# Kernel tuning notes

Hardware: AMD Instinct MI355X
Metric: run time of the kernel (lower is better)

Reference implementation:

```python
import jax, jax.numpy as jnp
import numpy as np

K = 16  # nsample for knn_point

def _bn(x, g, b):
    # inference-mode BatchNorm1d folded to per-channel affine (running stats 0/1)
    return x * g[None, :, None] + b[None, :, None]

def _knn(xyz, k):
    # xyz: [B,3,N] -> idx [B,N,k] of k nearest neighbors (squared L2)
    p = xyz.transpose(0, 2, 1)                                   # [B,N,3]
    sq = jnp.sum(p * p, axis=-1)                                 # [B,N]
    d = sq[:, :, None] + sq[:, None, :] - 2.0 * jnp.einsum('bnc,bmc->bnm', p, p)
    _, idx = jax.lax.top_k(-d, k)
    return idx

def _gather(hT, idx):
    # hT: [B,N,C], idx: [B,N,K] -> [B,N,K,C]
    return jax.vmap(lambda a, i: a[i])(hT, idx)

def setup_inputs():
    key = jax.random.key(0)
    ks = jax.random.split(key, 12)
    B, N, C = 16, 2048, 128
    def w(k, shape, fan):
        return jax.random.normal(k, shape, jnp.float32) * (1.0 / np.sqrt(fan))
    o = jnp.ones; z = jnp.zeros
    return {
        'points': jax.random.normal(ks[0], (B, 6, N), jnp.float32),
        'label': jax.random.uniform(ks[1], (B, 1, 16), jnp.float32),
        'We1': w(ks[2], (C, 6), 6), 'ge1': o(C), 'be1': z(C),
        'We2': w(ks[3], (C, C), C), 'ge2': o(C), 'be2': z(C),
        'W1': w(ks[4], (3, C, C), C), 'g1': o((3, C)), 'b1': z((3, C)),
        'W2': w(ks[5], (3, C, C), C), 'g2': o((3, C)), 'b2': z((3, C)),
        'Wf': w(ks[6], (1024, 3 * C), 3 * C), 'gf': o(1024), 'bf': z(1024),
        'Wl': w(ks[7], (64, 16), 16), 'gl': o(64), 'bl': z(64),
        'Wc1': w(ks[8], (512, 3136), 3136), 'bc1': z(512), 'gc1': o(512), 'bb1': z(512),
        'Wc2': w(ks[9], (256, 512), 512), 'bc2': z(256), 'gc2': o(256), 'bb2': z(256),
        'Wc3': w(ks[10], (50, 256), 256), 'bc3': z(50),
    }

def reference(points, label, We1, ge1, be1, We2, ge2, be2, W1, g1, b1, W2, g2, b2,
              Wf, gf, bf, Wl, gl, bl, Wc1, bc1, gc1, bb1, Wc2, bc2, gc2, bb2, Wc3, bc3):
    B, _, N = points.shape
    x = points[:, :6, :]
    xyz = x[:, :3, :]
    idx = _knn(xyz, K)                                            # [B,N,16]
    # input embedding: two conv1x1 + BN + ReLU
    h = jax.nn.relu(_bn(jnp.einsum('oc,bcn->bon', We1, x), ge1, be1))
    h = jax.nn.relu(_bn(jnp.einsum('oc,bcn->bon', We2, h), ge2, be2))
    xs = []
    for i in range(3):  # PVDSA_Res blocks (simplified: conv-BN-ReLU, kNN max-agg, conv-BN + residual)
        t = jax.nn.relu(_bn(jnp.einsum('oc,bcn->bon', W1[i], h), g1[i], b1[i]))
        nbr = _gather(t.transpose(0, 2, 1), idx)                  # [B,N,K,C]
        m = nbr.max(axis=2).transpose(0, 2, 1)                    # [B,C,N]
        h = jax.nn.relu(_bn(jnp.einsum('oc,bcn->bon', W2[i], m), g2[i], b2[i]) + h)
        xs.append(h)
    xcat = jnp.concatenate(xs, axis=1)                            # [B,384,N]
    xf = jax.nn.leaky_relu(_bn(jnp.einsum('oc,bcn->bon', Wf, xcat), gf, bf), 0.2)  # [B,1024,N]
    x_max = xf.max(axis=-1)                                       # [B,1024]
    x_avg = xf.mean(axis=-1)                                      # [B,1024]
    cls = jnp.broadcast_to(label.transpose(0, 2, 1), (B, 16, N))
    lab = jax.nn.leaky_relu(_bn(jnp.einsum('oc,bcn->bon', Wl, cls), gl, bl), 0.2)  # [B,64,N]
    glob = jnp.concatenate([
        jnp.broadcast_to(x_max[:, :, None], (B, 1024, N)),
        jnp.broadcast_to(x_avg[:, :, None], (B, 1024, N)),
        lab], axis=1)
    xa = jnp.concatenate([xf, glob], axis=1)                      # [B,3136,N]
    c = jax.nn.relu(_bn(jnp.einsum('oc,bcn->bon', Wc1, xa) + bc1[None, :, None], gc1, bb1))
    c = jax.nn.relu(_bn(jnp.einsum('oc,bcn->bon', Wc2, c) + bc2[None, :, None], gc2, bb2))
    out = jnp.einsum('oc,bcn->bon', Wc3, c) + bc3[None, :, None]  # [B,50,N]
    return out
```

## Files before the change

kernel.cpp:

```cpp
#include <hip/hip_runtime.h>
#include <cstdint>
#include <cstddef>

#define DEVINL __device__ __forceinline__

typedef float    f32x4 __attribute__((ext_vector_type(4)));
typedef _Float16 f16x8 __attribute__((ext_vector_type(8)));
typedef _Float16 f16x4 __attribute__((ext_vector_type(4)));

constexpr int BB = 16, NN = 2048, MM = 32768;

constexpr size_t OFF_WE1 = 0;
constexpr size_t OFF_WE2 = OFF_WE1 + 128 * 64 * 2;
constexpr size_t OFF_W1  = OFF_WE2 + 128 * 128 * 2;
constexpr size_t OFF_W2  = OFF_W1  + 3 * 128 * 128 * 2;
constexpr size_t OFF_WF  = OFF_W2  + 3 * 128 * 128 * 2;
constexpr size_t OFF_WC1 = OFF_WF  + 1024 * 384 * 2;
constexpr size_t OFF_WC2 = OFF_WC1 + 512 * 1024 * 2;
constexpr size_t OFF_WC3 = OFF_WC2 + 256 * 512 * 2;
constexpr size_t OFF_BC2 = OFF_WC3 + 128 * 256 * 2;
constexpr size_t OFF_BC3 = OFF_BC2 + 256 * 4;
constexpr size_t OFF_CVEC= OFF_BC3 + 128 * 4;
constexpr size_t OFF_PMAX= OFF_CVEC+ 16 * 512 * 4;
constexpr size_t OFF_PSUM= OFF_PMAX+ 16 * 16 * 1024 * 4;
constexpr size_t OFF_IDX = OFF_PSUM+ 16 * 16 * 1024 * 4;
constexpr size_t OFF_R1  = 8ull << 20;
constexpr size_t OFF_X0  = OFF_R1;
constexpr size_t OFF_HT  = OFF_R1 + (4ull  << 20);
constexpr size_t OFF_TT  = OFF_R1 + (12ull << 20);
constexpr size_t OFF_MT  = OFF_R1 + (20ull << 20);
constexpr size_t OFF_C1  = OFF_R1;
constexpr size_t OFF_XCAT= OFF_R1 + (32ull << 20);
constexpr size_t OFF_C2  = OFF_XCAT;
constexpr size_t OFF_XF  = OFF_XCAT + (24ull << 20);

__global__ __launch_bounds__(256) void fold_all_kernel(
    const float* We1, const float* ge1, const float* We2, const float* ge2,
    const float* W1,  const float* g1,  const float* W2,  const float* g2,
    const float* Wf,  const float* gf,  const float* Wc1, const float* gc1,
    const float* Wc2, const float* gc2, const float* Wc3,
    const float* gc2b, const float* bc2, const float* bb2, const float* bc3,
    const float* pts, char* ws)
{
    const int bid = blockIdx.x;
    const int tid = threadIdx.x;

    if (bid == 4704) {
        ((float*)(ws + OFF_BC2))[tid] = gc2b[tid] * bc2[tid] + bb2[tid];
        return;
    }
    if (bid == 4705) {
        if (tid < 128) ((float*)(ws + OFF_BC3))[tid] = (tid < 50) ? bc3[tid] : 0.f;
        return;
    }
    if (bid >= 4706) {
        int m = (bid - 4706) * 256 + tid;
        int b = m >> 11, n = m & 2047;
        const float* ps = pts + (size_t)b * 6 * 2048 + n;
        _Float16 tmp[64];
#pragma unroll
        for (int c = 0; c < 64; ++c) tmp[c] = (_Float16)0.f;
#pragma unroll
        for (int c = 0; c < 6; ++c) tmp[c] = (_Float16)ps[(size_t)c << 11];
        _Float16* dst = (_Float16*)(ws + OFF_X0) + (size_t)m * 64;
#pragma unroll
        for (int v = 0; v < 8; ++v) *(f16x8*)(dst + v * 8) = *(const f16x8*)(tmp + v * 8);
        return;
    }

    int id, base;
    if      (bid < 32)   { id = 0;  base = 0;    }
    else if (bid < 96)   { id = 1;  base = 32;   }
    else if (bid < 160)  { id = 2;  base = 96;   }
    else if (bid < 224)  { id = 3;  base = 160;  }
    else if (bid < 288)  { id = 4;  base = 224;  }
    else if (bid < 352)  { id = 5;  base = 288;  }
    else if (bid < 416)  { id = 6;  base = 352;  }
    else if (bid < 480)  { id = 7;  base = 416;  }
    else if (bid < 2016) { id = 8;  base = 480;  }
    else if (bid < 4064) { id = 9;  base = 2016; }
    else if (bid < 4576) { id = 10; base = 4064; }
    else                 { id = 11; base = 4576; }

    const float* src = nullptr; const float* g = nullptr; _Float16* dst = nullptr;
    int O = 0, K = 0, lds = 0, Kp = 0;
    switch (id) {
        case 0:  src = We1; g = ge1; O = 128; K = 6;    lds = 6;    Kp = 64;   dst = (_Float16*)(ws + OFF_WE1); break;
        case 1:  src = We2; g = ge2; O = 128; K = 128;  lds = 128;  Kp = 128;  dst = (_Float16*)(ws + OFF_WE2); break;
        case 2: case 3: case 4: {
            int i = id - 2;
            src = W1 + (size_t)i * 16384; g = g1 + i * 128; O = 128; K = 128; lds = 128; Kp = 128;
            dst = (_Float16*)(ws + OFF_W1) + (size_t)i * 16384; break; }
        case 5: case 6: case 7: {
            int i = id - 5;
            src = W2 + (size_t)i * 16384; g = g2 + i * 128; O = 128; K = 128; lds = 128; Kp = 128;
            dst = (_Float16*)(ws + OFF_W2) + (size_t)i * 16384; break; }
        case 8:  src = Wf;  g = gf;  O = 1024; K = 384;  lds = 384;  Kp = 384;  dst = (_Float16*)(ws + OFF_WF);  break;
        case 9:  src = Wc1; g = gc1; O = 512;  K = 1024; lds = 3136; Kp = 1024; dst = (_Float16*)(ws + OFF_WC1); break;
        case 10: src = Wc2; g = gc2; O = 256;  K = 512;  lds = 512;  Kp = 512;  dst = (_Float16*)(ws + OFF_WC2); break;
        default: src = Wc3; g = nullptr; O = 50; K = 256; lds = 256; Kp = 256;  dst = (_Float16*)(ws + OFF_WC3); break;
    }
    int e = (bid - base) * 256 + tid;
    int o = e / Kp, k = e - o * Kp;
    float v = 0.f;
    if (o < O && k < K) {
        v = src[(size_t)o * lds + k];
        if (g) v *= g[o];
    }
    dst[e] = (_Float16)v;
}

DEVINL float knn_dist(const float4 pq, const float4 pm) {
    float t = pq.x * pm.x;
    t = fmaf(pq.y, pm.y, t);
    t = fmaf(pq.z, pm.z, t);
    return fmaf(-2.f, t, pm.w);
}

#define KNN_DINS(X) do { \
    const float x_ = (X); \
    d15 = __builtin_amdgcn_fmed3f(x_, d14, d15); \
    d14 = __builtin_amdgcn_fmed3f(x_, d13, d14); \
    d13 = __builtin_amdgcn_fmed3f(x_, d12, d13); \
    d12 = __builtin_amdgcn_fmed3f(x_, d11, d12); \
    d11 = __builtin_amdgcn_fmed3f(x_, d10, d11); \
    d10 = __builtin_amdgcn_fmed3f(x_, d9,  d10); \
    d9  = __builtin_amdgcn_fmed3f(x_, d8,  d9);  \
    d8  = __builtin_amdgcn_fmed3f(x_, d7,  d8);  \
    d7  = __builtin_amdgcn_fmed3f(x_, d6,  d7);  \
    d6  = __builtin_amdgcn_fmed3f(x_, d5,  d6);  \
    d5  = __builtin_amdgcn_fmed3f(x_, d4,  d5);  \
    d4  = __builtin_amdgcn_fmed3f(x_, d3,  d4);  \
    d3  = __builtin_amdgcn_fmed3f(x_, d2,  d3);  \
    d2  = __builtin_amdgcn_fmed3f(x_, d1,  d2);  \
    d1  = __builtin_amdgcn_fmed3f(x_, d0,  d1);  \
    d0  = __builtin_amdgcn_fmed3f(x_, -3.4e38f, d0); \
} while (0)

#define KNN_CE(A, B) { const float lo_ = fminf(A, B), hi_ = fmaxf(A, B); A = lo_; B = hi_; }

#define KNN_MERGE(OFF) do { \
    const float n0  = __shfl_xor(d0,  OFF), n1  = __shfl_xor(d1,  OFF), \
                n2  = __shfl_xor(d2,  OFF), n3  = __shfl_xor(d3,  OFF), \
                n4  = __shfl_xor(d4,  OFF), n5  = __shfl_xor(d5,  OFF), \
                n6  = __shfl_xor(d6,  OFF), n7  = __shfl_xor(d7,  OFF), \
                n8  = __shfl_xor(d8,  OFF), n9  = __shfl_xor(d9,  OFF), \
                n10 = __shfl_xor(d10, OFF), n11 = __shfl_xor(d11, OFF), \
                n12 = __shfl_xor(d12, OFF), n13 = __shfl_xor(d13, OFF), \
                n14 = __shfl_xor(d14, OFF), n15 = __shfl_xor(d15, OFF); \
    d0  = fminf(d0,  n15); d1  = fminf(d1,  n14); d2  = fminf(d2,  n13); d3  = fminf(d3,  n12); \
    d4  = fminf(d4,  n11); d5  = fminf(d5,  n10); d6  = fminf(d6,  n9);  d7  = fminf(d7,  n8);  \
    d8  = fminf(d8,  n7);  d9  = fminf(d9,  n6);  d10 = fminf(d10, n5);  d11 = fminf(d11, n4);  \
    d12 = fminf(d12, n3);  d13 = fminf(d13, n2);  d14 = fminf(d14, n1);  d15 = fminf(d15, n0);  \
    KNN_CE(d0, d8)  KNN_CE(d1, d9)  KNN_CE(d2, d10) KNN_CE(d3, d11) \
    KNN_CE(d4, d12) KNN_CE(d5, d13) KNN_CE(d6, d14) KNN_CE(d7, d15) \
    KNN_CE(d0, d4)  KNN_CE(d1, d5)  KNN_CE(d2, d6)  KNN_CE(d3, d7)  \
    KNN_CE(d8, d12) KNN_CE(d9, d13) KNN_CE(d10,d14) KNN_CE(d11,d15) \
    KNN_CE(d0, d2)  KNN_CE(d1, d3)  KNN_CE(d4, d6)  KNN_CE(d5, d7)  \
    KNN_CE(d8, d10) KNN_CE(d9, d11) KNN_CE(d12,d14) KNN_CE(d13,d15) \
    KNN_CE(d0, d1)  KNN_CE(d2, d3)  KNN_CE(d4, d5)  KNN_CE(d6, d7)  \
    KNN_CE(d8, d9)  KNN_CE(d10,d11) KNN_CE(d12,d13) KNN_CE(d14,d15) \
} while (0)

__global__ __launch_bounds__(256) void knn_kernel(const float* __restrict__ pts, int* __restrict__ idxout)
{
    __shared__ float4 P[2048];
    __shared__ unsigned short buf[32][96];
    __shared__ int cnt[32];
    __shared__ int wcnt[32];
    const int tid = threadIdx.x;
    const int b = blockIdx.x;
    const float* pb = pts + (size_t)b * 6 * 2048;
    for (int i = tid; i < 2048; i += 256) {
        float x = pb[i];
        float y = pb[2048 + i];
        float z = pb[4096 + i];
        P[i] = make_float4(x, y, z, x * x + y * y + z * z);
    }
    if (tid < 32) { cnt[tid] = 0; wcnt[tid] = 0; }
    __syncthreads();

    const int p = tid & 7;
    const int g = tid >> 3;
    const int q = blockIdx.y * 32 + g;
    const float4 pq = P[q];

    float d0 = 3.4e38f, d1 = 3.4e38f, d2 = 3.4e38f, d3 = 3.4e38f;
#pragma unroll 4
    for (int it = 0; it < 256; ++it) {
        const float4 pm = P[it * 8 + p];
        const float x = knn_dist(pq, pm);
        d3 = __builtin_amdgcn_fmed3f(x, d2, d3);
        d2 = __builtin_amdgcn_fmed3f(x, d1, d2);
        d1 = __builtin_amdgcn_fmed3f(x, d0, d1);
        d0 = fminf(x, d0);
    }
    float d4 = 3.4e38f, d5 = 3.4e38f, d6 = 3.4e38f, d7 = 3.4e38f,
          d8 = 3.4e38f, d9 = 3.4e38f, d10 = 3.4e38f, d11 = 3.4e38f,
          d12 = 3.4e38f, d13 = 3.4e38f, d14 = 3.4e38f, d15 = 3.4e38f;
    KNN_MERGE(1);
    KNN_MERGE(2);
    KNN_MERGE(4);
    const float tub = d15;

#pragma unroll 4
    for (int it = 0; it < 256; ++it) {
        const int m = it * 8 + p;
        const float d = knn_dist(pq, P[m]);
        if (d <= tub) {
            const int pos = atomicAdd(&cnt[g], 1);
            if (pos < 96) buf[g][pos] = (unsigned short)m;
        }
    }
    int C = cnt[g];
    if (C > 96) C = 96;

    d0 = 3.4e38f; d1 = 3.4e38f; d2 = 3.4e38f; d3 = 3.4e38f;
    d4 = 3.4e38f; d5 = 3.4e38f; d6 = 3.4e38f; d7 = 3.4e38f;
    d8 = 3.4e38f; d9 = 3.4e38f; d10 = 3.4e38f; d11 = 3.4e38f;
    d12 = 3.4e38f; d13 = 3.4e38f; d14 = 3.4e38f; d15 = 3.4e38f;
    for (int j = p; j < C; j += 8) {
        const int m = buf[g][j];
        const float x = knn_dist(pq, P[m]);
        KNN_DINS(x);
    }
    KNN_MERGE(1);
    KNN_MERGE(2);
    KNN_MERGE(4);
    const float t = d15;

    int* op = idxout + (((size_t)(b << 11) + q) << 4);
    for (int j = p; j < C; j += 8) {
        const int m = buf[g][j];
        const float d = knn_dist(pq, P[m]);
        if (d <= t) {
            const int pos = atomicAdd(&wcnt[g], 1);
            if (pos < 16) op[pos] = m;
        }
    }
}

template<int TM>
__global__ __launch_bounds__(256) void gemm_tile(
    const _Float16* __restrict__ W, const _Float16* __restrict__ X,
    _Float16* __restrict__ Y, float* __restrict__ Y32,
    const float* __restrict__ bias, const _Float16* __restrict__ Res,
    int Kp, int ldX, int xoff, int ldY, int yoff, int Opad,
    int act, int biasPerBatch, int ldR, int roff, int Olimit,
    float* __restrict__ pmax, float* __restrict__ psum)
{
    constexpr int MI = TM / 32;
    constexpr int ASZ = 128 * 64;
    constexpr int BSZ = TM * 64;
    __shared__ _Float16 SH[2 * (ASZ + BSZ)];

    const int tid  = threadIdx.x;
    const int lane = tid & 63, wave = tid >> 6;
    const int r = lane & 15, quad = lane >> 4;
    const int m_blk = blockIdx.x * TM, o_blk = blockIdx.y * 128;
    const int oh = (wave >> 1) * 64, mh = (wave & 1) * (TM / 2);

    f32x4 acc[4][MI];
#pragma unroll
    for (int a = 0; a < 4; ++a)
#pragma unroll
        for (int c = 0; c < MI; ++c) acc[a][c] = (f32x4){0.f, 0.f, 0.f, 0.f};

    const int srow  = wave * 8 + (lane >> 3);
    const int sslot = lane & 7;

    auto STAGE = [&](int bufi, int k0) {
        _Float16* As = SH + bufi * (ASZ + BSZ);
        _Float16* Bs = As + ASZ;
#pragma unroll
        for (int t = 0; t < 4; ++t) {
            const int rowA = t * 32 + srow;
            const int gk = k0 + ((sslot ^ (rowA & 7)) << 3);
            const _Float16* gA = W + (size_t)(o_blk + rowA) * Kp + gk;
            __builtin_amdgcn_global_load_lds(
                (const __attribute__((address_space(1))) unsigned int*)gA,
                (__attribute__((address_space(3))) unsigned int*)(As + t * 2048 + wave * 512),
                16, 0, 0);
        }
#pragma unroll
        for (int t = 0; t < TM / 32; ++t) {
            const int rowB = t * 32 + srow;
            const int gk = k0 + ((sslot ^ (rowB & 7)) << 3);
            const _Float16* gB = X + (size_t)(m_blk + rowB) * ldX + xoff + gk;
            __builtin_amdgcn_global_load_lds(
                (const __attribute__((address_space(1))) unsigned int*)gB,
                (__attribute__((address_space(3))) unsigned int*)(Bs + t * 2048 + wave * 512),
                16, 0, 0);
        }
    };

    const int nt = Kp >> 6;
    STAGE(0, 0);
    int cur = 0;
    for (int t = 0; t < nt; ++t) {
        if (t + 1 < nt) {
            STAGE(cur ^ 1, (t + 1) << 6);
            if constexpr (TM == 128) asm volatile("s_waitcnt vmcnt(8)" ::: "memory");
            else                     asm volatile("s_waitcnt vmcnt(6)" ::: "memory");
        } else {
            asm volatile("s_waitcnt vmcnt(0)" ::: "memory");
        }
        __builtin_amdgcn_sched_barrier(0);
        __builtin_amdgcn_s_barrier();
        asm volatile("" ::: "memory");

        const _Float16* As = SH + cur * (ASZ + BSZ);
        const _Float16* Bs = As + ASZ;
        __builtin_amdgcn_s_setprio(1);
#pragma unroll
        for (int ks = 0; ks < 2; ++ks) {
            f16x8 af[4], bf[MI];
#pragma unroll
            for (int oi = 0; oi < 4; ++oi) {
                const int row = oh + oi * 16 + r;
                const int slot = (ks * 4 + quad) ^ (row & 7);
                af[oi] = *(const f16x8*)(As + row * 64 + slot * 8);
            }
#pragma unroll
            for (int mi = 0; mi < MI; ++mi) {
                const int row = mh + mi * 16 + r;
                const int slot = (ks * 4 + quad) ^ (row & 7);
                bf[mi] = *(const f16x8*)(Bs + row * 64 + slot * 8);
            }
#pragma unroll
            for (int oi = 0; oi < 4; ++oi)
#pragma unroll
                for (int mi = 0; mi < MI; ++mi)
                    acc[oi][mi] = __builtin_amdgcn_mfma_f32_16x16x32_f16(af[oi], bf[mi], acc[oi][mi], 0, 0, 0);
        }
        __builtin_amdgcn_s_setprio(0);
        asm volatile("" ::: "memory");
        __builtin_amdgcn_s_barrier();
        cur ^= 1;
    }

    const int bb = biasPerBatch ? (m_blk >> 11) * Opad : 0;
    __syncthreads();

    if (Y32) {
#pragma unroll
        for (int oi = 0; oi < 4; ++oi) {
            const int og = o_blk + oh + oi * 16 + quad * 4;
            const f32x4 bv = *(const f32x4*)(bias + bb + og);
#pragma unroll
            for (int mi = 0; mi < MI; ++mi) {
                const int m = m_blk + mh + mi * 16 + r;
                const int bidx = m >> 11, n = m & 2047;
                f32x4 v = acc[oi][mi] + bv;
#pragma unroll
                for (int j = 0; j < 4; ++j) {
                    float x = v[j];
                    if (act == 1)      x = (x > 0.f) ? x : 0.0f;
                    else if (act == 2) x = (x > 0.f) ? x : 0.2f * x;
                    const int o = og + j;
                    if (o < Olimit)
                        Y32[((size_t)(bidx * 50 + o) << 11) + n] = x;
                }
            }
        }
        return;
    }

    _Float16* OT = SH;
#pragma unroll
    for (int oi = 0; oi < 4; ++oi) {
        const int ol = oh + oi * 16 + quad * 4;
        const f32x4 bv = *(const f32x4*)(bias + bb + o_blk + ol);
#pragma unroll
        for (int mi = 0; mi < MI; ++mi) {
            const int row = mh + mi * 16 + r;
            f32x4 v = acc[oi][mi] + bv;
            if (Res) {
                f16x4 rr = *(const f16x4*)(Res + (size_t)(m_blk + row) * ldR + roff + o_blk + ol);
#pragma unroll
                for (int j = 0; j < 4; ++j) v[j] += (float)rr[j];
            }
            f16x4 ov;
#pragma unroll
            for (int j = 0; j < 4; ++j) {
                float x = v[j];
                if (act == 1)      x = (x > 0.f) ? x : 0.0f;
                else if (act == 2) x = (x > 0.f) ? x : 0.2f * x;
                ov[j] = (_Float16)x;
            }
            const int s = ((ol >> 2) ^ (row & 31)) << 2;
            *(f16x4*)(OT + row * 128 + s) = ov;
        }
    }
    __syncthreads();
#pragma unroll
    for (int it2 = 0; it2 < TM / 16; ++it2) {
        const int row = it2 * 16 + (tid >> 4);
        const int c = tid & 15;
        const int s0 = ((c * 2) ^ (row & 31)) << 2;
        const int s1 = ((c * 2 + 1) ^ (row & 31)) << 2;
        f16x4 a = *(const f16x4*)(OT + row * 128 + s0);
        f16x4 b2 = *(const f16x4*)(OT + row * 128 + s1);
        f16x8 o8;
        o8[0] = a[0]; o8[1] = a[1]; o8[2] = a[2]; o8[3] = a[3];
        o8[4] = b2[0]; o8[5] = b2[1]; o8[6] = b2[2]; o8[7] = b2[3];
        *(f16x8*)(Y + (size_t)(m_blk + row) * ldY + yoff + o_blk + c * 8) = o8;
    }

    if constexpr (TM == 128) {
        if (pmax) {
            const int cg = tid & 31, h = tid >> 5;
            float mx0 = -3.4e38f, mx1 = -3.4e38f, mx2 = -3.4e38f, mx3 = -3.4e38f;
            float sm0 = 0.f, sm1 = 0.f, sm2 = 0.f, sm3 = 0.f;
#pragma unroll
            for (int rr = 0; rr < 16; ++rr) {
                const int r2 = h * 16 + rr;
                const f16x4 v = *(const f16x4*)(OT + r2 * 128 + ((cg ^ (r2 & 31)) << 2));
                const float x0 = (float)v[0], x1 = (float)v[1], x2 = (float)v[2], x3 = (float)v[3];
                mx0 = fmaxf(mx0, x0); sm0 += x0;
                mx1 = fmaxf(mx1, x1); sm1 += x1;
                mx2 = fmaxf(mx2, x2); sm2 += x2;
                mx3 = fmaxf(mx3, x3); sm3 += x3;
            }
            __syncthreads();
            float* PR = (float*)SH;
            float* pw = PR + (size_t)(h * 128 + cg * 4) * 2;
            pw[0] = mx0; pw[1] = sm0; pw[2] = mx1; pw[3] = sm1;
            pw[4] = mx2; pw[5] = sm2; pw[6] = mx3; pw[7] = sm3;
            __syncthreads();
            if (tid < 128) {
                float M = -3.4e38f, S = 0.f;
#pragma unroll
                for (int h2 = 0; h2 < 8; ++h2) {
                    M = fmaxf(M, PR[(size_t)(h2 * 128 + tid) * 2]);
                    S += PR[(size_t)(h2 * 128 + tid) * 2 + 1];
                }
                const int b2 = m_blk >> 11, mt = (m_blk >> 7) & 15;
                pmax[((size_t)(b2 * 16 + mt) << 10) + o_blk + tid] = M;
                psum[((size_t)(b2 * 16 + mt) << 10) + o_blk + tid] = S;
            }
        }
    }
}

typedef short s16x8 __attribute__((ext_vector_type(8)));
__global__ __launch_bounds__(256) void gather_max_kernel(
    const short* __restrict__ T, const int* __restrict__ idx, short* __restrict__ Mo)
{
    const int tid = threadIdx.x;
    const int p = blockIdx.x * 16 + (tid >> 4);
    const int l = tid & 15;
    const int b = p >> 11;
    const int* ip = idx + (size_t)p * 16;
    size_t row = (size_t)((b << 11) + ip[0]);
    s16x8 cur = *(const s16x8*)(T + row * 128 + l * 8);
    unsigned short best[8];
#pragma unroll
    for (int e = 0; e < 8; ++e) best[e] = (unsigned short)cur[e];
#pragma unroll
    for (int j = 1; j < 16; ++j) {
        row = (size_t)((b << 11) + ip[j]);
        s16x8 v = *(const s16x8*)(T + row * 128 + l * 8);
#pragma unroll
        for (int e = 0; e < 8; ++e) {
            unsigned short u = (unsigned short)v[e];
            if (u > best[e]) best[e] = u;
        }
    }
    s16x8 ov;
#pragma unroll
    for (int e = 0; e < 8; ++e) ov[e] = (short)best[e];
    *(s16x8*)(Mo + (size_t)p * 128 + l * 8) = ov;
}

__global__ __launch_bounds__(256) void cvec_kernel(
    const float* __restrict__ label, const float* __restrict__ Wl, const float* __restrict__ gl, const float* __restrict__ bl,
    const float* __restrict__ Wc1, const float* __restrict__ bc1, const float* __restrict__ gc1, const float* __restrict__ bb1,
    const float* __restrict__ pmax, const float* __restrict__ psum, float* __restrict__ cvec)
{
    __shared__ float v[2112];
    __shared__ float red[256];
    const int b = blockIdx.x, og = blockIdx.y, tid = threadIdx.x;
    for (int i = tid; i < 1024; i += 256) {
        float mx = -3.4e38f, sm = 0.f;
#pragma unroll
        for (int c = 0; c < 16; ++c) {
            mx = fmaxf(mx, pmax[((size_t)(b * 16 + c) << 10) + i]);
            sm += psum[((size_t)(b * 16 + c) << 10) + i];
        }
        v[i] = mx;
        v[1024 + i] = sm * (1.f / 2048.f);
    }
    if (tid < 64) {
        float s = 0.f;
        for (int i = 0; i < 16; ++i) s += Wl[tid * 16 + i] * label[b * 16 + i];
        s = gl[tid] * s + bl[tid];
        v[2048 + tid] = (s > 0.f) ? s : 0.2f * s;
    }
    __syncthreads();
    const int o = og * 64 + (tid >> 2), part = tid & 3;
    const float* wrow = Wc1 + (size_t)o * 3136 + 1024 + part * 528;
    float s = 0.f;
    for (int j = 0; j < 528; ++j) s += wrow[j] * v[part * 528 + j];
    red[tid] = s;
    __syncthreads();
    if (part == 0) {
        float tot = red[tid] + red[tid + 1] + red[tid + 2] + red[tid + 3];
        cvec[((size_t)b << 9) + o] = gc1[o] * (tot + bc1[o]) + bb1[o];
    }
}

extern "C" void kernel_launch(void* const* d_in, const int* in_sizes, int n_in,
                              void* d_out, int out_size, void* d_ws, size_t ws_size,
                              hipStream_t stream)
{
    (void)in_sizes; (void)n_in; (void)out_size; (void)ws_size;
    const float* points = (const float*)d_in[0];
    const float* label  = (const float*)d_in[1];
    const float* We1 = (const float*)d_in[2];
    const float* ge1 = (const float*)d_in[3];
    const float* be1 = (const float*)d_in[4];
    const float* We2 = (const float*)d_in[5];
    const float* ge2 = (const float*)d_in[6];
    const float* be2 = (const float*)d_in[7];
    const float* W1  = (const float*)d_in[8];
    const float* g1  = (const float*)d_in[9];
    const float* b1  = (const float*)d_in[10];
    const float* W2  = (const float*)d_in[11];
    const float* g2  = (const float*)d_in[12];
    const float* b2  = (const float*)d_in[13];
    const float* Wf  = (const float*)d_in[14];
    const float* gf  = (const float*)d_in[15];
    const float* bfv = (const float*)d_in[16];
    const float* Wl  = (const float*)d_in[17];
    const float* gl  = (const float*)d_in[18];
    const float* bl  = (const float*)d_in[19];
    const float* Wc1 = (const float*)d_in[20];
    const float* bc1 = (const float*)d_in[21];
    const float* gc1 = (const float*)d_in[22];
    const float* bb1 = (const float*)d_in[23];
    const float* Wc2 = (const float*)d_in[24];
    const float* bc2 = (const float*)d_in[25];
    const float* gc2 = (const float*)d_in[26];
    const float* bb2 = (const float*)d_in[27];
    const float* Wc3 = (const float*)d_in[28];
    const float* bc3 = (const float*)d_in[29];

    char* ws = (char*)d_ws;
    _Float16* hT  = (_Float16*)(ws + OFF_HT);
    _Float16* tT  = (_Float16*)(ws + OFF_TT);
    _Float16* mT  = (_Float16*)(ws + OFF_MT);
    _Float16* xct = (_Float16*)(ws + OFF_XCAT);
    _Float16* xf  = (_Float16*)(ws + OFF_XF);
    _Float16* c1  = (_Float16*)(ws + OFF_C1);
    _Float16* c2  = (_Float16*)(ws + OFF_C2);
    int*      idx = (int*)     (ws + OFF_IDX);
    _Float16* x0  = (_Float16*)(ws + OFF_X0);

    _Float16* wE1 = (_Float16*)(ws + OFF_WE1);
    _Float16* wE2 = (_Float16*)(ws + OFF_WE2);
    _Float16* w1f = (_Float16*)(ws + OFF_W1);
    _Float16* w2f = (_Float16*)(ws + OFF_W2);
    _Float16* wF  = (_Float16*)(ws + OFF_WF);
    _Float16* wC1 = (_Float16*)(ws + OFF_WC1);
    _Float16* wC2 = (_Float16*)(ws + OFF_WC2);
    _Float16* wC3 = (_Float16*)(ws + OFF_WC3);
    float* bC2 = (float*)(ws + OFF_BC2);
    float* bC3 = (float*)(ws + OFF_BC3);
    float* cv  = (float*)(ws + OFF_CVEC);
    float* pmx = (float*)(ws + OFF_PMAX);
    float* psm = (float*)(ws + OFF_PSUM);

    fold_all_kernel<<<dim3(4834), 256, 0, stream>>>(We1, ge1, We2, ge2, W1, g1, W2, g2,
                                                    Wf, gf, Wc1, gc1, Wc2, gc2, Wc3,
                                                    gc2, bc2, bb2, bc3, points, ws);
    knn_kernel<<<dim3(BB, NN / 32), 256, 0, stream>>>(points, idx);

    gemm_tile<64><<<dim3(512, 1), 256, 0, stream>>>(wE1, x0, tT, nullptr, be1, nullptr, 64, 64, 0, 128, 0, 128, 1, 0, 0, 0, 128, nullptr, nullptr);
    gemm_tile<64><<<dim3(512, 1), 256, 0, stream>>>(wE2, tT, hT, nullptr, be2, nullptr, 128, 128, 0, 128, 0, 128, 1, 0, 0, 0, 128, nullptr, nullptr);

    for (int i = 0; i < 3; ++i) {
        const _Float16* hin = (i == 0) ? hT : xct;
        int ldH  = (i == 0) ? 128 : 384;
        int offH = (i == 0) ? 0 : (i - 1) * 128;
        gemm_tile<64><<<dim3(512, 1), 256, 0, stream>>>(w1f + (size_t)i * 16384, hin, tT, nullptr, b1 + i * 128, nullptr,
                                                        128, ldH, offH, 128, 0, 128, 1, 0, 0, 0, 128, nullptr, nullptr);
        gather_max_kernel<<<dim3(MM / 16), 256, 0, stream>>>((const short*)tT, idx, (short*)mT);
        gemm_tile<64><<<dim3(512, 1), 256, 0, stream>>>(w2f + (size_t)i * 16384, mT, xct, nullptr, b2 + i * 128, hin,
                                                        128, 128, 0, 384, i * 128, 128, 1, 0, ldH, offH, 128, nullptr, nullptr);
    }

    gemm_tile<128><<<dim3(256, 8), 256, 0, stream>>>(wF, xct, xf, nullptr, bfv, nullptr, 384, 384, 0, 1024, 0, 1024, 2, 0, 0, 0, 1024, pmx, psm);

    cvec_kernel<<<dim3(BB, 8), 256, 0, stream>>>(label, Wl, gl, bl, Wc1, bc1, gc1, bb1, pmx, psm, cv);

    gemm_tile<128><<<dim3(256, 4), 256, 0, stream>>>(wC1, xf, c1, nullptr, cv, nullptr, 1024, 1024, 0, 512, 0, 512, 1, 1, 0, 0, 512, nullptr, nullptr);
    gemm_tile<128><<<dim3(256, 2), 256, 0, stream>>>(wC2, c1, c2, nullptr, bC2, nullptr, 512, 512, 0, 256, 0, 256, 1, 0, 0, 0, 256, nullptr, nullptr);
    gemm_tile<128><<<dim3(256, 1), 256, 0, stream>>>(wC3, c2, nullptr, (float*)d_out, bC3, nullptr, 256, 256, 0, 0, 0, 128, 0, 0, 0, 0, 50, nullptr, nullptr);
}
```

Before: 414.6 us.

## Add 256x256 LDS-pipelined GEMM kernel for the two largest layers

Adds a new 512-thread GEMM kernel with 256x256 output tiles. It loads global memory straight into LDS with a fine-grained double-buffered schedule, explicit vmcnt waits and raised priority around the MFMA work. The kernel is used for the 1024x384 feature layer, including the fused max/sum partial reductions, and for the 512x1024 classifier layer. The larger tiles cut redundant operand traffic and raise MFMA density. In exchange the kernel needs 128KB of LDS per block and gets fewer blocks per GPU (512 and 256), and the partial-reduction layout changes to 8 chunks per batch.

```diff
diff --git a/kernel.cpp b/kernel.cpp
--- a/kernel.cpp
+++ b/kernel.cpp
@@ -240,14 +240,181 @@
     }
 }
 
+__global__ __launch_bounds__(512, 2) void gemm256(
+    const _Float16* __restrict__ W, const _Float16* __restrict__ X,
+    _Float16* __restrict__ Y, const float* __restrict__ bias,
+    int Kp, int ldX, int ldY, int Opad, int act, int biasPerBatch,
+    float* __restrict__ pmax, float* __restrict__ psum)
+{
+    __shared__ _Float16 SH[65536];
+    const int tid  = threadIdx.x;
+    const int lane = tid & 63, wave = tid >> 6;
+    const int r = lane & 15, quad = lane >> 4;
+    const int wo = wave & 3, wm = wave >> 2;
+    const int m_blk = blockIdx.x * 256, o_blk = blockIdx.y * 256;
+    const int nt = Kp >> 6;
+
+    f32x4 acc[4][8];
+#pragma unroll
+    for (int a = 0; a < 4; ++a)
+#pragma unroll
+        for (int c = 0; c < 8; ++c) acc[a][c] = (f32x4){0.f, 0.f, 0.f, 0.f};
+
+    auto STAGE_HALF = [&](int mat, int tile, int h) {
+        const int d = tile & 1;
+        _Float16* base = SH + (size_t)(((d * 2 + mat) * 2 + h) << 13);
+#pragma unroll
+        for (int i = 0; i < 2; ++i) {
+            const int g  = ((wave * 2 + i) << 6) + lane;
+            const int R  = g >> 2, s2 = g & 3;
+            const int K4 = s2 ^ ((R >> 1) & 3);
+            const int gk = (tile << 6) + (h << 5) + (K4 << 3);
+            const _Float16* src = (mat == 0)
+                ? W + (size_t)(o_blk + R) * Kp + gk
+                : X + (size_t)(m_blk + R) * ldX + gk;
+            __builtin_amdgcn_global_load_lds(
+                (const __attribute__((address_space(1))) unsigned int*)src,
+                (__attribute__((address_space(3))) unsigned int*)(base + ((wave * 2 + i) << 9)),
+                16, 0, 0);
+        }
+    };
+
+    STAGE_HALF(0, 0, 0); STAGE_HALF(1, 0, 0);
+    STAGE_HALF(0, 0, 1); STAGE_HALF(1, 0, 1);
+    if (nt > 1) { STAGE_HALF(0, 1, 0); STAGE_HALF(1, 1, 0); }
+
+    f16x8 af[4];
+    for (int t = 0; t < nt; ++t) {
+        const int d = t & 1;
+#pragma unroll
+        for (int ph = 0; ph < 4; ++ph) {
+            const int ks = ph >> 1, mh = ph & 1;
+            if (ph == 0) {
+                if (t == nt - 1) asm volatile("s_waitcnt vmcnt(4)" ::: "memory");
+                else             asm volatile("s_waitcnt vmcnt(8)" ::: "memory");
+            } else if (ph == 2) {
+                if (t == nt - 1) asm volatile("s_waitcnt vmcnt(0)" ::: "memory");
+                else             asm volatile("s_waitcnt vmcnt(8)" ::: "memory");
+            }
+            __builtin_amdgcn_sched_barrier(0);
+            __builtin_amdgcn_s_barrier();
+            __builtin_amdgcn_sched_barrier(0);
+
+            if (mh == 0) {
+#pragma unroll
+                for (int oi = 0; oi < 4; ++oi) {
+                    const int R  = (wo << 6) + (oi << 4) + r;
+                    const int s2 = quad ^ ((R >> 1) & 3);
+                    af[oi] = *(const f16x8*)(SH + (size_t)(((d * 2 + 0) * 2 + ks) << 13)
+                                                + (size_t)(((R << 2) + s2) << 3));
+                }
+            }
+            f16x8 bf[4];
+#pragma unroll
+            for (int j = 0; j < 4; ++j) {
+                const int mi = (mh << 2) + j;
+                const int R  = (wm << 7) + (mi << 4) + r;
+                const int s2 = quad ^ ((R >> 1) & 3);
+                bf[j] = *(const f16x8*)(SH + (size_t)(((d * 2 + 1) * 2 + ks) << 13)
+                                            + (size_t)(((R << 2) + s2) << 3));
+            }
+
+            if (ph == 0)      { if (t + 1 < nt) STAGE_HALF(0, t + 1, 1); }
+            else if (ph == 1) { if (t + 1 < nt) STAGE_HALF(1, t + 1, 1); }
+            else if (ph == 2) { if (t + 2 < nt) STAGE_HALF(0, t + 2, 0); }
+            else              { if (t + 2 < nt) STAGE_HALF(1, t + 2, 0); }
+
+            __builtin_amdgcn_s_setprio(1);
+#pragma unroll
+            for (int oi = 0; oi < 4; ++oi)
+#pragma unroll
+                for (int j = 0; j < 4; ++j)
+                    acc[oi][(mh << 2) + j] =
+                        __builtin_amdgcn_mfma_f32_16x16x32_f16(af[oi], bf[j], acc[oi][(mh << 2) + j], 0, 0, 0);
+            __builtin_amdgcn_s_setprio(0);
+            __builtin_amdgcn_sched_barrier(0);
+        }
+    }
+    __syncthreads();
+
+    const int bb = biasPerBatch ? (m_blk >> 11) * Opad : 0;
+    _Float16* OT = SH;
+#pragma unroll
+    for (int oi = 0; oi < 4; ++oi) {
+        const int ol = (wo << 6) + (oi << 4) + (quad << 2);
+        const f32x4 bv = *(const f32x4*)(bias + bb + o_blk + ol);
+#pragma unroll
+        for (int mi = 0; mi < 8; ++mi) {
+            const int row = (wm << 7) + (mi << 4) + r;
+            f32x4 v = acc[oi][mi] + bv;
+            f16x4 ov;
+#pragma unroll
+            for (int j = 0; j < 4; ++j) {
+                float x = v[j];
+                if (act == 1)      x = (x > 0.f) ? x : 0.0f;
+                else if (act == 2) x = (x > 0.f) ? x : 0.2f * x;
+                ov[j] = (_Float16)x;
+            }
+            const int s = (ol >> 2) ^ (row & 31);
+            *(f16x4*)(OT + row * 256 + s * 4) = ov;
+        }
+    }
+    __syncthreads();
+#pragma unroll
+    for (int p2 = 0; p2 < 16; ++p2) {
+        const int g = (p2 << 9) + tid;
+        const int row = g >> 5, c = g & 31;
+        const int s0 = ((c << 1)) ^ (row & 31);
+        const int s1 = ((c << 1) | 1) ^ (row & 31);
+        f16x4 a  = *(const f16x4*)(OT + row * 256 + s0 * 4);
+        f16x4 b2 = *(const f16x4*)(OT + row * 256 + s1 * 4);
+        f16x8 o8;
+        o8[0] = a[0]; o8[1] = a[1]; o8[2] = a[2]; o8[3] = a[3];
+        o8[4] = b2[0]; o8[5] = b2[1]; o8[6] = b2[2]; o8[7] = b2[3];
+        *(f16x8*)(Y + (size_t)(m_blk + row) * ldY + o_blk + (c << 3)) = o8;
+    }
+
+    if (pmax) {
+        const int cg = tid & 63, h8 = tid >> 6;
+        float mx0 = -3.4e38f, mx1 = -3.4e38f, mx2 = -3.4e38f, mx3 = -3.4e38f;
+        float sm0 = 0.f, sm1 = 0.f, sm2 = 0.f, sm3 = 0.f;
+#pragma unroll
+        for (int rr = 0; rr < 32; ++rr) {
+            const int row = (h8 << 5) + rr;
+            const f16x4 v = *(const f16x4*)(OT + row * 256 + ((cg ^ (row & 31)) << 2));
+            const float x0 = (float)v[0], x1 = (float)v[1], x2 = (float)v[2], x3 = (float)v[3];
+            mx0 = fmaxf(mx0, x0); sm0 += x0;
+            mx1 = fmaxf(mx1, x1); sm1 += x1;
+            mx2 = fmaxf(mx2, x2); sm2 += x2;
+            mx3 = fmaxf(mx3, x3); sm3 += x3;
+        }
+        __syncthreads();
+        float* PR = (float*)SH;
+        float* pw = PR + (size_t)(((h8 << 8) + (cg << 2)) << 1);
+        pw[0] = mx0; pw[1] = sm0; pw[2] = mx1; pw[3] = sm1;
+        pw[4] = mx2; pw[5] = sm2; pw[6] = mx3; pw[7] = sm3;
+        __syncthreads();
+        if (tid < 256) {
+            float M = -3.4e38f, S = 0.f;
+#pragma unroll
+            for (int h2 = 0; h2 < 8; ++h2) {
+                M = fmaxf(M, PR[(size_t)(((h2 << 8) + tid) << 1)]);
+                S += PR[(size_t)(((h2 << 8) + tid) << 1) + 1];
+            }
+            const int b2 = m_blk >> 11, mt = (m_blk >> 8) & 7;
+            pmax[((size_t)((b2 << 3) + mt) << 10) + o_blk + tid] = M;
+            psum[((size_t)((b2 << 3) + mt) << 10) + o_blk + tid] = S;
+        }
+    }
+}
+
 template<int TM>
 __global__ __launch_bounds__(256) void gemm_tile(
     const _Float16* __restrict__ W, const _Float16* __restrict__ X,
     _Float16* __restrict__ Y, float* __restrict__ Y32,
     const float* __restrict__ bias, const _Float16* __restrict__ Res,
     int Kp, int ldX, int xoff, int ldY, int yoff, int Opad,
-    int act, int biasPerBatch, int ldR, int roff, int Olimit,
-    float* __restrict__ pmax, float* __restrict__ psum)
+    int act, int biasPerBatch, int ldR, int roff, int Olimit)
 {
     constexpr int MI = TM / 32;
     constexpr int ASZ = 128 * 64;
@@ -405,41 +572,6 @@
         o8[0] = a[0]; o8[1] = a[1]; o8[2] = a[2]; o8[3] = a[3];
         o8[4] = b2[0]; o8[5] = b2[1]; o8[6] = b2[2]; o8[7] = b2[3];
         *(f16x8*)(Y + (size_t)(m_blk + row) * ldY + yoff + o_blk + c * 8) = o8;
-    }
-
-    if constexpr (TM == 128) {
-        if (pmax) {
-            const int cg = tid & 31, h = tid >> 5;
-            float mx0 = -3.4e38f, mx1 = -3.4e38f, mx2 = -3.4e38f, mx3 = -3.4e38f;
-            float sm0 = 0.f, sm1 = 0.f, sm2 = 0.f, sm3 = 0.f;
-#pragma unroll
-            for (int rr = 0; rr < 16; ++rr) {
-                const int r2 = h * 16 + rr;
-                const f16x4 v = *(const f16x4*)(OT + r2 * 128 + ((cg ^ (r2 & 31)) << 2));
-                const float x0 = (float)v[0], x1 = (float)v[1], x2 = (float)v[2], x3 = (float)v[3];
-                mx0 = fmaxf(mx0, x0); sm0 += x0;
-                mx1 = fmaxf(mx1, x1); sm1 += x1;
-                mx2 = fmaxf(mx2, x2); sm2 += x2;
-                mx3 = fmaxf(mx3, x3); sm3 += x3;
-            }
-            __syncthreads();
-            float* PR = (float*)SH;
-            float* pw = PR + (size_t)(h * 128 + cg * 4) * 2;
-            pw[0] = mx0; pw[1] = sm0; pw[2] = mx1; pw[3] = sm1;
-            pw[4] = mx2; pw[5] = sm2; pw[6] = mx3; pw[7] = sm3;
-            __syncthreads();
-            if (tid < 128) {
-                float M = -3.4e38f, S = 0.f;
-#pragma unroll
-                for (int h2 = 0; h2 < 8; ++h2) {
-                    M = fmaxf(M, PR[(size_t)(h2 * 128 + tid) * 2]);
-                    S += PR[(size_t)(h2 * 128 + tid) * 2 + 1];
-                }
-                const int b2 = m_blk >> 11, mt = (m_blk >> 7) & 15;
-                pmax[((size_t)(b2 * 16 + mt) << 10) + o_blk + tid] = M;
-                psum[((size_t)(b2 * 16 + mt) << 10) + o_blk + tid] = S;
-            }
-        }
     }
 }
 
@@ -484,9 +616,9 @@
     for (int i = tid; i < 1024; i += 256) {
         float mx = -3.4e38f, sm = 0.f;
 #pragma unroll
-        for (int c = 0; c < 16; ++c) {
-            mx = fmaxf(mx, pmax[((size_t)(b * 16 + c) << 10) + i]);
-            sm += psum[((size_t)(b * 16 + c) << 10) + i];
+        for (int c = 0; c < 8; ++c) {
+            mx = fmaxf(mx, pmax[((size_t)(b * 8 + c) << 10) + i]);
+            sm += psum[((size_t)(b * 8 + c) << 10) + i];
         }
         v[i] = mx;
         v[1024 + i] = sm * (1.f / 2048.f);
@@ -576,25 +708,26 @@
                                                     gc2, bc2, bb2, bc3, points, ws);
     knn_kernel<<<dim3(BB, NN / 32), 256, 0, stream>>>(points, idx);
 
-    gemm_tile<64><<<dim3(512, 1), 256, 0, stream>>>(wE1, x0, tT, nullptr, be1, nullptr, 64, 64, 0, 128, 0, 128, 1, 0, 0, 0, 128, nullptr, nullptr);
-    gemm_tile<64><<<dim3(512, 1), 256, 0, stream>>>(wE2, tT, hT, nullptr, be2, nullptr, 128, 128, 0, 128, 0, 128, 1, 0, 0, 0, 128, nullptr, nullptr);
+    gemm_tile<64><<<dim3(512, 1), 256, 0, stream>>>(wE1, x0, tT, nullptr, be1, nullptr, 64, 64, 0, 128, 0, 128, 1, 0, 0, 0, 128);
+    gemm_tile<64><<<dim3(512, 1), 256, 0, stream>>>(wE2, tT, hT, nullptr, be2, nullptr, 128, 128, 0, 128, 0, 128, 1, 0, 0, 0, 128);
 
     for (int i = 0; i < 3; ++i) {
         const _Float16* hin = (i == 0) ? hT : xct;
         int ldH  = (i == 0) ? 128 : 384;
         int offH = (i == 0) ? 0 : (i - 1) * 128;
         gemm_tile<64><<<dim3(512, 1), 256, 0, stream>>>(w1f + (size_t)i * 16384, hin, tT, nullptr, b1 + i * 128, nullptr,
-                                                        128, ldH, offH, 128, 0, 128, 1, 0, 0, 0, 128, nullptr, nullptr);
+                                                        128, ldH, offH, 128, 0, 128, 1, 0, 0, 0, 128);
         gather_max_kernel<<<dim3(MM / 16), 256, 0, stream>>>((const short*)tT, idx, (short*)mT);
         gemm_tile<64><<<dim3(512, 1), 256, 0, stream>>>(w2f + (size_t)i * 16384, mT, xct, nullptr, b2 + i * 128, hin,
-                                                        128, 128, 0, 384, i * 128, 128, 1, 0, ldH, offH, 128, nullptr, nullptr);
-    }
-
-    gemm_tile<128><<<dim3(256, 8), 256, 0, stream>>>(wF, xct, xf, nullptr, bfv, nullptr, 384, 384, 0, 1024, 0, 1024, 2, 0, 0, 0, 1024, pmx, psm);
+                                                        128, 128, 0, 384, i * 128, 128, 1, 0, ldH, offH, 128);
+    }
+
+    gemm256<<<dim3(128, 4), 512, 0, stream>>>(wF, xct, xf, bfv, 384, 384, 1024, 1024, 2, 0, pmx, psm);
 
     cvec_kernel<<<dim3(BB, 8), 256, 0, stream>>>(label, Wl, gl, bl, Wc1, bc1, gc1, bb1, pmx, psm, cv);
 
-    gemm_tile<128><<<dim3(256, 4), 256, 0, stream>>>(wC1, xf, c1, nullptr, cv, nullptr, 1024, 1024, 0, 512, 0, 512, 1, 1, 0, 0, 512, nullptr, nullptr);
-    gemm_tile<128><<<dim3(256, 2), 256, 0, stream>>>(wC2, c1, c2, nullptr, bC2, nullptr, 512, 512, 0, 256, 0, 256, 1, 0, 0, 0, 256, nullptr, nullptr);
-    gemm_tile<128><<<dim3(256, 1), 256, 0, stream>>>(wC3, c2, nullptr, (float*)d_out, bC3, nullptr, 256, 256, 0, 0, 0, 128, 0, 0, 0, 0, 50, nullptr, nullptr);
+    gemm256<<<dim3(128, 2), 512, 0, stream>>>(wC1, xf, c1, cv, 1024, 1024, 512, 512, 1, 1, nullptr, nullptr);
+
+    gemm_tile<128><<<dim3(256, 2), 256, 0, stream>>>(wC2, c1, c2, nullptr, bC2, nullptr, 512, 512, 0, 256, 0, 256, 1, 0, 0, 0, 256);
+    gemm_tile<128><<<dim3(256, 1), 256, 0, stream>>>(wC3, c2, nullptr, (float*)d_out, bC3, nullptr, 256, 256, 0, 0, 0, 128, 0, 0, 0, 0, 50);
 }
```

After: 397.6 us. 4.1% less time.
